# Performance work log

Measured on AMD Instinct MI355X. Metric: run time of the kernel, lower is better.

## Reference

```python
import jax, jax.numpy as jnp
import numpy as np
from jax import lax

RADIUS = 0.25
K = 32          # num_neighbors
S = 2048        # num_centers
GROUPS = 8      # GroupNorm groups
EPS = 1e-5


def setup_inputs() -> dict:
    key = jax.random.key(0)
    ks = jax.random.split(key, 8)
    B, N, C = 8, 8192, 64
    inp = {
        "coords": jax.random.normal(ks[0], (B, 3, N), jnp.float32),
        "features": jax.random.normal(ks[1], (B, C, N), jnp.float32),
    }
    chans = [C + 3, 64, 64, 128]  # +3 for included relative coordinates
    for i in range(3):
        inp[f"w{i}"] = jax.random.normal(ks[2 + i], (chans[i + 1], chans[i]), jnp.float32) * 0.02
        inp[f"b{i}"] = jnp.zeros((chans[i + 1],), jnp.float32)
        inp[f"g{i}"] = jnp.ones((chans[i + 1],), jnp.float32)
        inp[f"be{i}"] = jnp.zeros((chans[i + 1],), jnp.float32)
    return inp


def _fps(coords, num_centers):
    # coords: [B,3,N] -> indices [B,S] via iterative farthest point sampling
    pts = jnp.transpose(coords, (0, 2, 1))  # [B,N,3]
    B, N, _ = pts.shape
    init_idx = jnp.zeros((B,), jnp.int32)
    init_mind = jnp.full((B, N), 1e10, jnp.float32)

    def step(carry, _):
        mind, last = carry
        lastpt = jnp.take_along_axis(pts, last[:, None, None], axis=1)  # [B,1,3]
        d = jnp.sum((pts - lastpt) ** 2, axis=-1)  # [B,N]
        mind = jnp.minimum(mind, d)
        nxt = jnp.argmax(mind, axis=-1).astype(jnp.int32)
        return (mind, nxt), nxt

    (_, _), rest = lax.scan(step, (init_mind, init_idx), None, length=num_centers - 1)
    idx = jnp.concatenate([init_idx[None, :], rest], axis=0)  # [S,B]
    return jnp.transpose(idx)  # [B,S]


def _ball_query(centers, pts, radius, k):
    # centers [B,3,S], pts [B,3,N] -> neighbor indices [B,S,k] (first-k-in-order, pad with first hit)
    cn = jnp.sum(centers**2, axis=1)                     # [B,S]
    pn = jnp.sum(pts**2, axis=1)                         # [B,N]
    cp = jnp.einsum('bds,bdn->bsn', centers, pts)        # [B,S,N]
    d2 = cn[:, :, None] + pn[:, None, :] - 2.0 * cp      # [B,S,N]
    mask = d2 < radius * radius
    order = jnp.argsort(jnp.logical_not(mask), axis=-1, stable=True)  # in-ball indices first, in index order
    idx = order[:, :, :k]
    cnt = jnp.sum(mask, axis=-1)                         # [B,S]
    slot_ok = jnp.arange(k)[None, None, :] < cnt[:, :, None]
    idx = jnp.where(slot_ok, idx, idx[:, :, :1])         # pad with first found index
    idx = jnp.where(cnt[:, :, None] > 0, idx, 0)         # empty ball -> index 0 (matches CUDA default)
    return idx


def _group(x, idx):
    # x [B,C,N], idx [B,S,K] -> [B,C,S,K]
    return jax.vmap(lambda f, i: f[:, i])(x, idx)


def _groupnorm(x, gamma, beta):
    B, C, Sx, Kx = x.shape
    xr = x.reshape(B, GROUPS, C // GROUPS, Sx, Kx)
    mu = jnp.mean(xr, axis=(2, 3, 4), keepdims=True)
    var = jnp.var(xr, axis=(2, 3, 4), keepdims=True)
    xr = (xr - mu) * lax.rsqrt(var + EPS)
    x = xr.reshape(B, C, Sx, Kx)
    return x * gamma[None, :, None, None] + beta[None, :, None, None]


def reference(coords, features, w0, b0, g0, be0, w1, b1, g1, be1, w2, b2, g2, be2):
    center_idx = _fps(coords, S)                                  # [B,S]
    centers = jax.vmap(lambda c, i: c[:, i])(coords, center_idx)  # [B,3,S]
    nidx = _ball_query(centers, coords, RADIUS, K)                # [B,S,K]
    ncoords = _group(coords, nidx) - centers[:, :, :, None]       # [B,3,S,K]
    x = jnp.concatenate([ncoords, _group(features, nidx)], axis=1)  # [B,67,S,K]
    for w, b, g, be in ((w0, b0, g0, be0), (w1, b1, g1, be1), (w2, b2, g2, be2)):
        x = jnp.einsum('oi,bisk->bosk', w, x) + b[None, :, None, None]  # 1x1 conv2d
        x = _groupnorm(x, g, be)
        x = x * jax.nn.sigmoid(x)  # Swish
    return jnp.max(x, axis=-1)     # [B,128,S]
```

## Files before the change

kernel.cpp:

```cpp
#include <hip/hip_runtime.h>
#include <math.h>

#define BATCH 8
#define NPTS 8192
#define CFEAT 64
#define NC 2048
#define KNN 32
#define NSCOL (NC*KNN)
#define R2 0.0625f
#define GN_EPS 1e-5f
#define SBINS 32

#define OFF_CIDX   0ull
#define OFF_NIDX   65536ull
#define OFF_CENT   2162688ull
#define OFF_STATSP 2359296ull
#define OFF_STATSF 2408448ull
#define OFF_WT     2410496ull
#define OFF_XALL   4194304ull
#define OFF_Y      23068672ull
#define WS_NEEDED  (OFF_Y + 8ull*64*NSCOL*4ull)

static __device__ __forceinline__ unsigned f2bf(float f) {
    unsigned u = __float_as_uint(f);
    return (u + 0x7fffu + ((u >> 16) & 1u)) >> 16;
}

__global__ void prep_kernel(const float* __restrict__ w0, const float* __restrict__ w1,
                            const float* __restrict__ w2, float* __restrict__ statsP,
                            float* __restrict__ statsF, float* __restrict__ wt)
{
    const int t = blockIdx.x * 256 + threadIdx.x;
    if (t < 3 * SBINS * 128) statsP[t] = 0.f;
    if (t < 384) statsF[t] = 0.f;
    if (t < 64 * 67) { int o = t / 67, i = t - o * 67; wt[i * 64 + o] = w0[t]; }
    if (t < 64 * 64) { int o = t >> 6, i = t & 63;     wt[4288 + i * 64 + o] = w1[t]; }
    if (t < 128 * 64){ int o = t >> 6, i = t & 63;     wt[8384 + i * 128 + o] = w2[t]; }
}

__global__ void reduce_stats(const float* __restrict__ statsPL, float* __restrict__ statsFL)
{
    const int t = threadIdx.x;
    if (t < 128) {
        float s = 0.f;
#pragma unroll
        for (int bin = 0; bin < SBINS; ++bin) s += statsPL[bin * 128 + t];
        statsFL[t] = s;
    }
}

__global__ __launch_bounds__(256) void build_xall(const float* __restrict__ coords,
                                                  const float* __restrict__ feats,
                                                  float* __restrict__ xall)
{
    const int tid = blockIdx.x * 256 + threadIdx.x;
    const int b = tid >> 13, p = tid & (NPTS - 1);
    const float* cb = coords + (size_t)b * 3 * NPTS;
    const float* fb = feats + (size_t)b * CFEAT * NPTS;
    float* xp = xall + (size_t)tid * 68;
    xp[0] = cb[p]; xp[1] = cb[NPTS + p]; xp[2] = cb[2 * NPTS + p];
#pragma unroll
    for (int c = 0; c < CFEAT; ++c) xp[3 + c] = fb[c * NPTS + p];
    xp[67] = 0.f;
}

__global__ __launch_bounds__(512) void fps_kernel(const float* __restrict__ coords,
                                                  int* __restrict__ cidx)
{
    extern __shared__ float smem[];
    float* sx = smem;
    float* sy = smem + NPTS;
    float* sz = smem + 2 * NPTS;
    unsigned long long* wpack = (unsigned long long*)(smem + 3 * NPTS);

    const int b = blockIdx.x;
    const int t = threadIdx.x;
    const float* cb = coords + (size_t)b * 3 * NPTS;

    float X[16], Y[16], Z[16], mind[16];
#pragma unroll
    for (int j = 0; j < 16; ++j) {
        int p = t + j * 512;
        X[j] = cb[p];
        Y[j] = cb[NPTS + p];
        Z[j] = cb[2 * NPTS + p];
        sx[p] = X[j]; sy[p] = Y[j]; sz[p] = Z[j];
        mind[j] = 1e10f;
    }
    if (t == 0) cidx[b * NC] = 0;
    __syncthreads();

    int cur = 0;
    for (int it = 1; it < NC; ++it) {
        const float lx = sx[cur], ly = sy[cur], lz = sz[cur];
        float bv = -1.0f; int bi = 0;
#pragma unroll
        for (int j = 0; j < 16; ++j) {
            float dx = __fsub_rn(X[j], lx);
            float dy = __fsub_rn(Y[j], ly);
            float dz = __fsub_rn(Z[j], lz);
            float d  = __fadd_rn(__fadd_rn(__fmul_rn(dx, dx), __fmul_rn(dy, dy)),
                                 __fmul_rn(dz, dz));
            float nm = fminf(mind[j], d);
            mind[j] = nm;
            if (nm > bv) { bv = nm; bi = t + j * 512; }
        }
        unsigned long long pack = ((unsigned long long)__float_as_uint(bv) << 32)
                                | (unsigned long long)(unsigned)(NPTS - 1 - bi);
#pragma unroll
        for (int o = 32; o > 0; o >>= 1) {
            unsigned long long other = __shfl_xor(pack, o);
            if (other > pack) pack = other;
        }
        unsigned long long* wp = wpack + (it & 1) * 8;
        if ((t & 63) == 0) wp[t >> 6] = pack;
        __syncthreads();
        unsigned long long best = wp[0];
#pragma unroll
        for (int w = 1; w < 8; ++w) {
            unsigned long long v = wp[w];
            if (v > best) best = v;
        }
        cur = NPTS - 1 - (int)(best & 0xffffffffu);
        if (t == 0) cidx[b * NC + it] = cur;
    }
}

__global__ __launch_bounds__(256) void bq_kernel(const float* __restrict__ coords,
                                                 const int* __restrict__ cidx,
                                                 int* __restrict__ nidx,
                                                 float* __restrict__ centers)
{
    const int s = blockIdx.x, b = blockIdx.y, t = threadIdx.x;
    __shared__ int s_idx[KNN];
    __shared__ int s_pref[9];
    __shared__ float s_c[3];
    __shared__ float s_cn;
    const float* cb = coords + (size_t)b * 3 * NPTS;
    if (t == 0) {
        int ci = cidx[b * NC + s];
        float cx = cb[ci], cy = cb[NPTS + ci], cz = cb[2 * NPTS + ci];
        s_c[0] = cx; s_c[1] = cy; s_c[2] = cz;
        s_cn = __fadd_rn(__fadd_rn(__fmul_rn(cx, cx), __fmul_rn(cy, cy)),
                         __fmul_rn(cz, cz));
    }
    __syncthreads();
    const float cx = s_c[0], cy = s_c[1], cz = s_c[2], cn = s_cn;
    const int base = t * 32;
    int cnt = 0;
    for (int j = 0; j < 32; ++j) {
        int p = base + j;
        float x = cb[p], y = cb[NPTS + p], z = cb[2 * NPTS + p];
        float pn = __fadd_rn(__fadd_rn(__fmul_rn(x, x), __fmul_rn(y, y)), __fmul_rn(z, z));
        float cp = __fadd_rn(__fadd_rn(__fmul_rn(cx, x), __fmul_rn(cy, y)), __fmul_rn(cz, z));
        float d2 = __fsub_rn(__fadd_rn(cn, pn), __fmul_rn(2.0f, cp));
        if (d2 < R2) ++cnt;
    }
    const int lane = t & 63, wid = t >> 6;
    int incl = cnt;
    for (int o = 1; o < 64; o <<= 1) {
        int v = __shfl_up(incl, o);
        if (lane >= o) incl += v;
    }
    if (lane == 63) s_pref[wid] = incl;
    __syncthreads();
    int ex = incl - cnt;
    for (int w = 0; w < wid; ++w) ex += s_pref[w];
    if (t == 255) s_pref[8] = ex + cnt;
    if (ex < KNN && cnt > 0) {
        int slot = ex;
        for (int j = 0; j < 32 && slot < KNN; ++j) {
            int p = base + j;
            float x = cb[p], y = cb[NPTS + p], z = cb[2 * NPTS + p];
            float pn = __fadd_rn(__fadd_rn(__fmul_rn(x, x), __fmul_rn(y, y)), __fmul_rn(z, z));
            float cp = __fadd_rn(__fadd_rn(__fmul_rn(cx, x), __fmul_rn(cy, y)), __fmul_rn(cz, z));
            float d2 = __fsub_rn(__fadd_rn(cn, pn), __fmul_rn(2.0f, cp));
            if (d2 < R2) { s_idx[slot] = p; ++slot; }
        }
    }
    __syncthreads();
    const int total = s_pref[8];
    if (t < KNN) {
        int v = (total == 0) ? 0 : ((t < total) ? s_idx[t] : s_idx[0]);
        nidx[(b * NC + s) * KNN + t] = v;
    }
    if (t < 3) centers[(b * NC + s) * 3 + t] = s_c[t];
}

__global__ __launch_bounds__(256) void l1_kernel(const float* __restrict__ xall,
                                                 const int* __restrict__ nidx,
                                                 const float* __restrict__ centers,
                                                 const float* __restrict__ wt,
                                                 const float* __restrict__ b0,
                                                 float* __restrict__ Y,
                                                 float* __restrict__ statsPL)
{
    __shared__ float sw[67 * 64 + 64];
    __shared__ float xs[68 * 64];
    __shared__ float s_sum[8], s_sq[8];
    const int b = blockIdx.y, t = threadIdx.x;
    const int col = t & 63, q = t >> 6;
    const int n = blockIdx.x * 64 + col;
    for (int i = t; i < 67 * 64; i += 256) sw[i] = wt[i];
    if (t < 64) sw[67 * 64 + t] = b0[t];
    if (t < 8) { s_sum[t] = 0.f; s_sq[t] = 0.f; }
    const int s = n >> 5, k = n & 31;
    const int p = nidx[(b * NC + s) * KNN + k];
    const float4* xp4 = (const float4*)(xall + (size_t)(b * NPTS + p) * 68);
    const float* cc = centers + (size_t)(b * NC + s) * 3;
#pragma unroll
    for (int r = 0; r < 4; ++r) {
        float4 v = xp4[q * 4 + r];
        int ch = (q * 4 + r) * 4;
        if (ch == 0) { v.x -= cc[0]; v.y -= cc[1]; v.z -= cc[2]; }
        xs[(ch + 0) * 64 + col] = v.x;
        xs[(ch + 1) * 64 + col] = v.y;
        xs[(ch + 2) * 64 + col] = v.z;
        xs[(ch + 3) * 64 + col] = v.w;
    }
    if (q == 3) {
        float4 v = xp4[16];
        xs[64 * 64 + col] = v.x;
        xs[65 * 64 + col] = v.y;
        xs[66 * 64 + col] = v.z;
        xs[67 * 64 + col] = v.w;
    }
    __syncthreads();
    float acc[16];
#pragma unroll
    for (int o = 0; o < 16; ++o) acc[o] = sw[67 * 64 + q * 16 + o];
    for (int i = 0; i < 67; ++i) {
        float xv = xs[i * 64 + col];
        const float* wr = sw + i * 64 + q * 16;
#pragma unroll
        for (int o = 0; o < 16; ++o) acc[o] = fmaf(wr[o], xv, acc[o]);
    }
    float* yb = Y + (size_t)b * 64 * NSCOL + n;
#pragma unroll
    for (int o = 0; o < 16; ++o) yb[(size_t)(q * 16 + o) * NSCOL] = acc[o];
#pragma unroll
    for (int g = 0; g < 2; ++g) {
        float sv = 0.f, sq = 0.f;
#pragma unroll
        for (int j = 0; j < 8; ++j) { float vv = acc[g * 8 + j]; sv += vv; sq = fmaf(vv, vv, sq); }
#pragma unroll
        for (int o = 32; o > 0; o >>= 1) { sv += __shfl_xor(sv, o); sq += __shfl_xor(sq, o); }
        if ((t & 63) == 0) { atomicAdd(&s_sum[q * 2 + g], sv); atomicAdd(&s_sq[q * 2 + g], sq); }
    }
    __syncthreads();
    if (t < 16) {
        const int bin = blockIdx.x & (SBINS - 1);
        const int g = t >> 1, kk = t & 1;
        atomicAdd(&statsPL[bin * 128 + (b * 8 + g) * 2 + kk], kk ? s_sq[g] : s_sum[g]);
    }
}

__global__ __launch_bounds__(256) void l2_kernel(const float* __restrict__ wt1,
                                                 const float* __restrict__ b1,
                                                 const float* __restrict__ g0,
                                                 const float* __restrict__ be0,
                                                 const float* __restrict__ statsF_in,
                                                 float* __restrict__ statsPL,
                                                 float* __restrict__ Y)
{
    __shared__ float sw[64 * 64 + 64];
    __shared__ float xs[64 * 64];
    __shared__ float sA[64], sB[64];
    __shared__ float s_sum[8], s_sq[8];
    const int b = blockIdx.y, t = threadIdx.x;
    const int col = t & 63, q = t >> 6;
    const int n = blockIdx.x * 64 + col;
    for (int i = t; i < 64 * 64; i += 256) sw[i] = wt1[i];
    if (t < 64) {
        sw[64 * 64 + t] = b1[t];
        const int g = t >> 3;
        const float inv = 1.0f / (8.0f * NSCOL);
        float mu = statsF_in[(b * 8 + g) * 2 + 0] * inv;
        float var = statsF_in[(b * 8 + g) * 2 + 1] * inv - mu * mu;
        float A = (1.0f / sqrtf(var + GN_EPS)) * g0[t];
        sA[t] = A; sB[t] = be0[t] - mu * A;
    }
    if (t < 8) { s_sum[t] = 0.f; s_sq[t] = 0.f; }
    __syncthreads();
    float* yb = Y + (size_t)b * 64 * NSCOL + n;
#pragma unroll
    for (int r = 0; r < 16; ++r) {
        int i = q * 16 + r;
        float raw = yb[(size_t)i * NSCOL];
        float v = fmaf(raw, sA[i], sB[i]);
        xs[i * 64 + col] = v * __builtin_amdgcn_rcpf(1.0f + __expf(-v));
    }
    __syncthreads();
    float acc[16];
#pragma unroll
    for (int o = 0; o < 16; ++o) acc[o] = sw[64 * 64 + q * 16 + o];
    for (int i = 0; i < 64; ++i) {
        float xv = xs[i * 64 + col];
        const float* wr = sw + i * 64 + q * 16;
#pragma unroll
        for (int o = 0; o < 16; ++o) acc[o] = fmaf(wr[o], xv, acc[o]);
    }
#pragma unroll
    for (int o = 0; o < 16; ++o) yb[(size_t)(q * 16 + o) * NSCOL] = acc[o];
#pragma unroll
    for (int g = 0; g < 2; ++g) {
        float sv = 0.f, sq = 0.f;
#pragma unroll
        for (int j = 0; j < 8; ++j) { float vv = acc[g * 8 + j]; sv += vv; sq = fmaf(vv, vv, sq); }
#pragma unroll
        for (int o = 32; o > 0; o >>= 1) { sv += __shfl_xor(sv, o); sq += __shfl_xor(sq, o); }
        if ((t & 63) == 0) { atomicAdd(&s_sum[q * 2 + g], sv); atomicAdd(&s_sq[q * 2 + g], sq); }
    }
    __syncthreads();
    if (t < 16) {
        const int bin = blockIdx.x & (SBINS - 1);
        const int g = t >> 1, kk = t & 1;
        atomicAdd(&statsPL[bin * 128 + (b * 8 + g) * 2 + kk], kk ? s_sq[g] : s_sum[g]);
    }
}

__global__ __launch_bounds__(256) void l3_kernel(const float* __restrict__ wt2,
                                                 const float* __restrict__ b2,
                                                 const float* __restrict__ g1,
                                                 const float* __restrict__ be1,
                                                 const float* __restrict__ statsF_in,
                                                 float* __restrict__ statsPL,
                                                 float* __restrict__ Y)
{
    __shared__ float sw[64 * 128 + 128];
    __shared__ float xs[64 * 64];
    __shared__ float sA[64], sB[64];
    __shared__ float s_sum[8], s_sq[8];
    const int b = blockIdx.y, t = threadIdx.x;
    const int col = t & 63, q = t >> 6;
    const int n = blockIdx.x * 64 + col;
    for (int i = t; i < 64 * 128; i += 256) sw[i] = wt2[i];
    if (t < 128) sw[64 * 128 + t] = b2[t];
    if (t < 64) {
        const int g = t >> 3;
        const float inv = 1.0f / (8.0f * NSCOL);
        float mu = statsF_in[(b * 8 + g) * 2 + 0] * inv;
        float var = statsF_in[(b * 8 + g) * 2 + 1] * inv - mu * mu;
        float A = (1.0f / sqrtf(var + GN_EPS)) * g1[t];
        sA[t] = A; sB[t] = be1[t] - mu * A;
    }
    if (t < 8) { s_sum[t] = 0.f; s_sq[t] = 0.f; }
    __syncthreads();
    float* yb = Y + (size_t)b * 64 * NSCOL + n;
#pragma unroll
    for (int r = 0; r < 16; ++r) {
        int i = q * 16 + r;
        float raw = yb[(size_t)i * NSCOL];
        float v = fmaf(raw, sA[i], sB[i]);
        xs[i * 64 + col] = v * __builtin_amdgcn_rcpf(1.0f + __expf(-v));
    }
    __syncthreads();
    float acc[32];
#pragma unroll
    for (int o = 0; o < 32; ++o) acc[o] = sw[64 * 128 + q * 32 + o];
    for (int i = 0; i < 64; ++i) {
        float xv = xs[i * 64 + col];
        const float* wr = sw + i * 128 + q * 32;
#pragma unroll
        for (int o = 0; o < 32; ++o) acc[o] = fmaf(wr[o], xv, acc[o]);
    }
#pragma unroll
    for (int g = 0; g < 2; ++g) {
        float sv = 0.f, sq = 0.f;
#pragma unroll
        for (int j = 0; j < 16; ++j) { float vv = acc[g * 16 + j]; sv += vv; sq = fmaf(vv, vv, sq); }
#pragma unroll
        for (int o = 32; o > 0; o >>= 1) { sv += __shfl_xor(sv, o); sq += __shfl_xor(sq, o); }
        if ((t & 63) == 0) { atomicAdd(&s_sum[q * 2 + g], sv); atomicAdd(&s_sq[q * 2 + g], sq); }
    }
    unsigned* yu = (unsigned*)yb;
#pragma unroll
    for (int j = 0; j < 16; ++j) {
        unsigned u = f2bf(acc[2 * j]) | (f2bf(acc[2 * j + 1]) << 16);
        yu[(size_t)(q * 16 + j) * NSCOL] = u;
    }
    __syncthreads();
    if (t < 16) {
        const int bin = blockIdx.x & (SBINS - 1);
        const int g = t >> 1, kk = t & 1;
        atomicAdd(&statsPL[bin * 128 + (b * 8 + g) * 2 + kk], kk ? s_sq[g] : s_sum[g]);
    }
}

__global__ __launch_bounds__(256) void fin_kernel(const unsigned* __restrict__ Yu,
                                                  const float* __restrict__ g2,
                                                  const float* __restrict__ be2,
                                                  const float* __restrict__ stats,
                                                  float* __restrict__ out)
{
    const int tid = blockIdx.x * 256 + threadIdx.x;
    const int s = tid & (NC - 1);
    const int cp = (tid >> 11) & 63;
    const int b = tid >> 17;
    const int g = cp >> 3;
    const float inv = 1.0f / (16.0f * NSCOL);
    float mu = stats[(b * 8 + g) * 2 + 0] * inv;
    float var = stats[(b * 8 + g) * 2 + 1] * inv - mu * mu;
    float rs = 1.0f / sqrtf(var + GN_EPS);
    const int c0 = cp * 2, c1 = c0 + 1;
    float A0 = rs * g2[c0], B0 = be2[c0] - mu * A0;
    float A1 = rs * g2[c1], B1 = be2[c1] - mu * A1;
    const unsigned* yb = Yu + (size_t)(b * 64 + cp) * NSCOL + s * KNN;
    float m0 = -INFINITY, m1 = -INFINITY;
#pragma unroll
    for (int qq = 0; qq < 8; ++qq) {
        uint4 v = ((const uint4*)yb)[qq];
        unsigned uu[4] = {v.x, v.y, v.z, v.w};
#pragma unroll
        for (int r = 0; r < 4; ++r) {
            float f0 = __uint_as_float(uu[r] << 16);
            float f1 = __uint_as_float(uu[r] & 0xffff0000u);
            float v0 = fmaf(f0, A0, B0);
            v0 = v0 * __builtin_amdgcn_rcpf(1.0f + __expf(-v0));
            m0 = fmaxf(m0, v0);
            float v1 = fmaf(f1, A1, B1);
            v1 = v1 * __builtin_amdgcn_rcpf(1.0f + __expf(-v1));
            m1 = fmaxf(m1, v1);
        }
    }
    out[(size_t)(b * 128 + c0) * NC + s] = m0;
    out[(size_t)(b * 128 + c1) * NC + s] = m1;
}

extern "C" void kernel_launch(void* const* d_in, const int* in_sizes, int n_in,
                              void* d_out, int out_size, void* d_ws, size_t ws_size,
                              hipStream_t stream)
{
    if (ws_size < WS_NEEDED) return;

    const float* coords = (const float*)d_in[0];
    const float* feats  = (const float*)d_in[1];
    const float* w0  = (const float*)d_in[2];
    const float* b0  = (const float*)d_in[3];
    const float* g0  = (const float*)d_in[4];
    const float* be0 = (const float*)d_in[5];
    const float* w1  = (const float*)d_in[6];
    const float* b1  = (const float*)d_in[7];
    const float* g1  = (const float*)d_in[8];
    const float* be1 = (const float*)d_in[9];
    const float* w2  = (const float*)d_in[10];
    const float* b2  = (const float*)d_in[11];
    const float* g2  = (const float*)d_in[12];
    const float* be2 = (const float*)d_in[13];
    float* out = (float*)d_out;

    char* ws = (char*)d_ws;
    int*   cidx    = (int*)(ws + OFF_CIDX);
    int*   nidx    = (int*)(ws + OFF_NIDX);
    float* centers = (float*)(ws + OFF_CENT);
    float* statsP  = (float*)(ws + OFF_STATSP);
    float* statsF  = (float*)(ws + OFF_STATSF);
    float* wt      = (float*)(ws + OFF_WT);
    float* xall    = (float*)(ws + OFF_XALL);
    float* Ybuf    = (float*)(ws + OFF_Y);

    prep_kernel<<<48, 256, 0, stream>>>(w0, w1, w2, statsP, statsF, wt);
    build_xall<<<(BATCH * NPTS) / 256, 256, 0, stream>>>(coords, feats, xall);
    fps_kernel<<<BATCH, 512, 3 * NPTS * 4 + 128, stream>>>(coords, cidx);
    bq_kernel<<<dim3(NC, BATCH), 256, 0, stream>>>(coords, cidx, nidx, centers);

    const dim3 lgrid(NSCOL / 64, BATCH);
    l1_kernel<<<lgrid, 256, 0, stream>>>(xall, nidx, centers, wt, b0, Ybuf, statsP);
    reduce_stats<<<1, 128, 0, stream>>>(statsP, statsF);
    l2_kernel<<<lgrid, 256, 0, stream>>>(wt + 4288, b1, g0, be0,
                                         statsF, statsP + SBINS * 128, Ybuf);
    reduce_stats<<<1, 128, 0, stream>>>(statsP + SBINS * 128, statsF + 128);
    l3_kernel<<<lgrid, 256, 0, stream>>>(wt + 8384, b2, g1, be1,
                                         statsF + 128, statsP + 2 * SBINS * 128, Ybuf);
    reduce_stats<<<1, 128, 0, stream>>>(statsP + 2 * SBINS * 128, statsF + 256);
    fin_kernel<<<(BATCH * 64 * NC) / 256, 256, 0, stream>>>(
        (const unsigned*)Ybuf, g2, be2, statsF + 256, out);
    (void)in_sizes; (void)n_in; (void)out_size;
}
```

Measured before the change: 3.092 ms.

## Widen FPS blocks to 1024 threads and fetch last point via scalar global load

The farthest-point-sampling kernel now uses 1024 threads per batch with 8 points per thread instead of 512 with 16, halving the serial per-thread work in each of the 2047 dependent iterations. The shared-memory coordinate copy is dropped, and the chosen point's coordinates are read from global memory through a wave-uniform index (readfirstlane), which should keep the load scalar and cached. The cross-wave reduction becomes a 16-lane shuffle butterfly rather than a sequential loop. In exchange there are more waves taking part in each barrier, and the global load sits on the critical path of every iteration.

```diff
diff --git a/kernel.cpp b/kernel.cpp
--- a/kernel.cpp
+++ b/kernel.cpp
@@ -64,38 +64,31 @@
     xp[67] = 0.f;
 }
 
-__global__ __launch_bounds__(512) void fps_kernel(const float* __restrict__ coords,
-                                                  int* __restrict__ cidx)
-{
-    extern __shared__ float smem[];
-    float* sx = smem;
-    float* sy = smem + NPTS;
-    float* sz = smem + 2 * NPTS;
-    unsigned long long* wpack = (unsigned long long*)(smem + 3 * NPTS);
+__global__ __launch_bounds__(1024) void fps_kernel(const float* __restrict__ coords,
+                                                   int* __restrict__ cidx)
+{
+    __shared__ unsigned long long s_pack[2][16];
 
     const int b = blockIdx.x;
     const int t = threadIdx.x;
     const float* cb = coords + (size_t)b * 3 * NPTS;
 
-    float X[16], Y[16], Z[16], mind[16];
-#pragma unroll
-    for (int j = 0; j < 16; ++j) {
-        int p = t + j * 512;
+    float X[8], Y[8], Z[8], mind[8];
+#pragma unroll
+    for (int j = 0; j < 8; ++j) {
+        const int p = t + j * 1024;
         X[j] = cb[p];
         Y[j] = cb[NPTS + p];
         Z[j] = cb[2 * NPTS + p];
-        sx[p] = X[j]; sy[p] = Y[j]; sz[p] = Z[j];
         mind[j] = 1e10f;
     }
     if (t == 0) cidx[b * NC] = 0;
-    __syncthreads();
-
-    int cur = 0;
+    float lx = cb[0], ly = cb[NPTS], lz = cb[2 * NPTS];
+
     for (int it = 1; it < NC; ++it) {
-        const float lx = sx[cur], ly = sy[cur], lz = sz[cur];
         float bv = -1.0f; int bi = 0;
 #pragma unroll
-        for (int j = 0; j < 16; ++j) {
+        for (int j = 0; j < 8; ++j) {
             float dx = __fsub_rn(X[j], lx);
             float dy = __fsub_rn(Y[j], ly);
             float dz = __fsub_rn(Z[j], lz);
@@ -103,26 +96,28 @@
                                  __fmul_rn(dz, dz));
             float nm = fminf(mind[j], d);
             mind[j] = nm;
-            if (nm > bv) { bv = nm; bi = t + j * 512; }
+            if (nm > bv) { bv = nm; bi = t + j * 1024; }
         }
         unsigned long long pack = ((unsigned long long)__float_as_uint(bv) << 32)
                                 | (unsigned long long)(unsigned)(NPTS - 1 - bi);
 #pragma unroll
         for (int o = 32; o > 0; o >>= 1) {
-            unsigned long long other = __shfl_xor(pack, o);
-            if (other > pack) pack = other;
+            unsigned long long op = __shfl_xor(pack, o);
+            if (op > pack) pack = op;
         }
-        unsigned long long* wp = wpack + (it & 1) * 8;
+        unsigned long long* wp = &s_pack[it & 1][0];
         if ((t & 63) == 0) wp[t >> 6] = pack;
         __syncthreads();
-        unsigned long long best = wp[0];
-#pragma unroll
-        for (int w = 1; w < 8; ++w) {
-            unsigned long long v = wp[w];
+        unsigned long long best = wp[t & 15];
+#pragma unroll
+        for (int o = 1; o < 16; o <<= 1) {
+            unsigned long long v = __shfl_xor(best, o);
             if (v > best) best = v;
         }
-        cur = NPTS - 1 - (int)(best & 0xffffffffu);
+        const int cur = NPTS - 1 - (int)(best & 0xffffffffu);
         if (t == 0) cidx[b * NC + it] = cur;
+        const int sc = __builtin_amdgcn_readfirstlane(cur);
+        lx = cb[sc]; ly = cb[NPTS + sc]; lz = cb[2 * NPTS + sc];
     }
 }
 
@@ -461,7 +456,7 @@
 
     prep_kernel<<<48, 256, 0, stream>>>(w0, w1, w2, statsP, statsF, wt);
     build_xall<<<(BATCH * NPTS) / 256, 256, 0, stream>>>(coords, feats, xall);
-    fps_kernel<<<BATCH, 512, 3 * NPTS * 4 + 128, stream>>>(coords, cidx);
+    fps_kernel<<<BATCH, 1024, 0, stream>>>(coords, cidx);
     bq_kernel<<<dim3(NC, BATCH), 256, 0, stream>>>(coords, cidx, nidx, centers);
 
     const dim3 lgrid(NSCOL / 64, BATCH);
```

Result: slower. 3.537 ms (+14.4%).
